# Kernel tuning notes

Measured on AMD Instinct MI355X. Metric: run time of the kernel, lower is better.

Reference implementation:

```python
import jax, jax.numpy as jnp
import numpy as np

N_NODES = 20000   # graph nodes (rows of x)
N_EDGES = 40000
NUM_ENT = 300000  # node_count: embedding table rows
EMB_DIM = 64
D = 2 * EMB_DIM           # self.emb_dim = 128
SE = int(0.36 * D)        # s_emb_dim = 46
TE = D - SE               # t_emb_dim = 82
F = 256                   # raw feature cols of x
HID = 128                 # n_hidden
OUT = 2


def setup_inputs() -> dict:
    key = jax.random.key(0)
    ks = jax.random.split(key, 24)
    def nrm(k, shape, fan_in):
        return jax.random.normal(k, shape, jnp.float32) / np.sqrt(fan_in)
    inp = {
        'x': jax.random.normal(ks[0], (N_NODES, F), jnp.float32),
        'heads': jax.random.randint(ks[1], (N_EDGES,), 0, NUM_ENT),
        'rels': jax.random.randint(ks[2], (N_EDGES,), 0, 4),
        'tails': jax.random.randint(ks[3], (N_EDGES,), 0, NUM_ENT),
        'weeks': jax.random.uniform(ks[4], (N_EDGES,), jnp.float32),
        'edge_src': jnp.sort(jax.random.randint(ks[5], (N_EDGES,), 0, N_NODES)),
        'edge_dst': jax.random.randint(ks[6], (N_EDGES,), 0, N_NODES),
        'node_type': jax.random.randint(ks[7], (N_NODES,), 0, 5),
        'edge_type': jax.random.randint(ks[8], (N_EDGES,), 0, 4),
        'edge_index': jax.random.randint(ks[9], (2, N_EDGES), 0, N_NODES),
        # learned parameters
        'ent_embs': nrm(ks[10], (NUM_ENT, SE), SE),
        'rel_embs': nrm(ks[11], (4, D), D),
        'w_freq': nrm(ks[12], (NUM_ENT, TE), TE),
        'w_phi': nrm(ks[13], (NUM_ENT, TE), TE),
        'w_amp': nrm(ks[14], (NUM_ENT, TE), TE),
        'Wih': nrm(ks[15], (4 * D, D), D),
        'Whh': nrm(ks[16], (4 * D, D), D),
        'bih': jnp.zeros((4 * D,), jnp.float32),
        'bhh': jnp.zeros((4 * D,), jnp.float32),
        'fc1_w': nrm(ks[17], (HID, F + D), F + D),
        'fc1_b': jnp.zeros((HID,), jnp.float32),
        'ln_g': jnp.ones((HID,), jnp.float32),
        'ln_b': jnp.zeros((HID,), jnp.float32),
        'out_w': nrm(ks[18], (OUT, HID), HID),
        'out_b': jnp.zeros((OUT,), jnp.float32),
    }
    return inp


def _lstm_last_per_segment(pre, seg, Whh, bhh):
    """Run one LSTM over edges sorted by seg, resetting state at group
    boundaries; return per-step hidden states and the scatter index that
    selects the last step of each group (others map to dummy row N_NODES).
    pre: [E, 4D] precomputed x @ Wih^T + bih (sorted by seg)."""
    reset = jnp.concatenate([jnp.ones((1,), bool), seg[1:] != seg[:-1]])
    def step(carry, inp):
        h, c = carry
        p, r = inp
        h = jnp.where(r, 0.0, h)
        c = jnp.where(r, 0.0, c)
        gates = p + h @ Whh.T + bhh
        i, f, g, o = jnp.split(gates, 4, axis=-1)
        c = jax.nn.sigmoid(f) * c + jax.nn.sigmoid(i) * jnp.tanh(g)
        h = jax.nn.sigmoid(o) * jnp.tanh(c)
        return (h, c), h
    zero = jnp.zeros((D,), pre.dtype)
    _, hs = jax.lax.scan(step, (zero, zero), (pre, reset))
    is_last = jnp.concatenate([seg[1:] != seg[:-1], jnp.ones((1,), bool)])
    idx = jnp.where(is_last, seg, N_NODES)  # dummy row for non-last steps
    return hs, idx


def reference(x, heads, rels, tails, weeks, edge_src, edge_dst, node_type,
              edge_type, edge_index, ent_embs, rel_embs, w_freq, w_phi, w_amp,
              Wih, Whh, bih, bhh, fc1_w, fc1_b, ln_g, ln_b, out_w, out_b):
    week = weeks.reshape(-1, 1)  # [E,1]
    # getEmbeddings: static entity emb + diachronic (amp*sin(freq*t+phi)) part
    h_t = w_amp[heads] * jnp.sin(w_freq[heads] * week + w_phi[heads])
    t_t = w_amp[tails] * jnp.sin(w_freq[tails] * week + w_phi[tails])
    h = jnp.concatenate([ent_embs[heads], h_t], axis=1)  # [E, D]
    t = jnp.concatenate([ent_embs[tails], t_t], axis=1)  # [E, D]
    r = rel_embs[rels]                                    # [E, D]
    scores = h * r * t                                    # [E, D]

    # Ragged per-group LSTM (src groups, then dst groups overwrite), fused
    # as a single segment-reset scan per pass. Input projection hoisted.
    pre = scores @ Wih.T + bih  # [E, 4D]
    emb = jnp.zeros((N_NODES + 1, D), scores.dtype)
    perm_s = jnp.argsort(edge_src)  # stable
    hs, idx = _lstm_last_per_segment(pre[perm_s], edge_src[perm_s], Whh, bhh)
    emb = emb.at[idx].set(hs)
    perm_d = jnp.argsort(edge_dst)
    hs, idx = _lstm_last_per_segment(pre[perm_d], edge_dst[perm_d], Whh, bhh)
    emb = emb.at[idx].set(hs)
    emb = emb[:N_NODES]

    # (hgtconv2 omitted: GeneralConv source unavailable; treated as identity)
    xc = jnp.concatenate([x, emb], axis=1)  # mask = arange(N): all rows
    h1 = xc @ fc1_w.T + fc1_b
    mu = jnp.mean(h1, axis=-1, keepdims=True)
    var = jnp.mean((h1 - mu) ** 2, axis=-1, keepdims=True)
    h1 = (h1 - mu) / jnp.sqrt(var + 1e-5) * ln_g + ln_b
    h1 = jax.nn.relu(h1)  # dropout: eval mode, identity
    return h1 @ out_w.T + out_b
```

## Files before the change

kernel.cpp:

```cpp
#include <hip/hip_runtime.h>
#include <math.h>

#define N_NODES 20000
#define N_EDGES 40000
#define SE 46
#define TE 82
#define NBLK 79

typedef short  s16x8 __attribute__((ext_vector_type(8)));
typedef short  s16x4 __attribute__((ext_vector_type(4)));
typedef float  f32x4 __attribute__((ext_vector_type(4)));

__device__ __forceinline__ float sigf(float x){ return 1.0f/(1.0f+__expf(-x)); }
__device__ __forceinline__ float tanh_f(float x){ return 1.0f - 2.0f/(__expf(2.0f*x)+1.0f); }
__device__ __forceinline__ int perm_out(int i){ return (i&3)*128 + (i>>2); }
__device__ __forceinline__ unsigned short f2bf(float f){
  unsigned u = __builtin_bit_cast(unsigned, f);
  unsigned r = (u + 0x7fff + ((u>>16)&1)) >> 16;
  return (unsigned short)r;
}
__device__ __forceinline__ float bf2f(short s){
  unsigned u = ((unsigned)(unsigned short)s) << 16;
  return __builtin_bit_cast(float, u);
}

#define GATHER_BLKS 2500
#define PREP_BLKS   704
#define HIST_BLKS   157
#define FRONT_BLKS  (GATHER_BLKS + PREP_BLKS + HIST_BLKS)

__global__ __launch_bounds__(256) void k_front(
    const int* __restrict__ heads, const int* __restrict__ rels,
    const int* __restrict__ tails, const float* __restrict__ weeks,
    const float* __restrict__ ent, const float* __restrict__ rel_embs,
    const float* __restrict__ wfreq, const float* __restrict__ wphi,
    const float* __restrict__ wamp, short* __restrict__ scores,
    const float* __restrict__ Wih, const float* __restrict__ Whh,
    const float* __restrict__ fc1w,
    short* __restrict__ WihB, short* __restrict__ WhhB2, short* __restrict__ fc1wbf,
    const int* __restrict__ esrc, const int* __restrict__ edst,
    int* __restrict__ scnt, int* __restrict__ dcnt){
  int blk = blockIdx.x, tid = threadIdx.x;
  if (blk < GATHER_BLKS){
    int c = blk*256 + tid;
    int e = c >> 4, d0 = (c & 15) << 3;
    int hd = heads[e], tl = tails[e], rl = rels[e];
    float wk = weeks[e];
    float hv[8], tv[8];
    if (d0 + 8 <= SE){
      const float* hp = ent + (size_t)hd*SE + d0;
      const float* tp = ent + (size_t)tl*SE + d0;
      #pragma unroll
      for (int j=0;j<4;j++){
        float2 a = *(const float2*)(hp + j*2); hv[2*j]=a.x; hv[2*j+1]=a.y;
        float2 b = *(const float2*)(tp + j*2); tv[2*j]=b.x; tv[2*j+1]=b.y;
      }
    } else if (d0 >= 48){
      int dt = d0 - SE;
      const float *hf = wfreq + (size_t)hd*TE + dt, *hp2 = wphi + (size_t)hd*TE + dt, *ha = wamp + (size_t)hd*TE + dt;
      const float *tf = wfreq + (size_t)tl*TE + dt, *tp2 = wphi + (size_t)tl*TE + dt, *ta = wamp + (size_t)tl*TE + dt;
      #pragma unroll
      for (int j=0;j<4;j++){
        float2 f_h = *(const float2*)(hf + j*2);
        float2 p_h = *(const float2*)(hp2 + j*2);
        float2 a_h = *(const float2*)(ha + j*2);
        float2 f_t = *(const float2*)(tf + j*2);
        float2 p_t = *(const float2*)(tp2 + j*2);
        float2 a_t = *(const float2*)(ta + j*2);
        hv[2*j]   = a_h.x*__sinf(f_h.x*wk + p_h.x);
        hv[2*j+1] = a_h.y*__sinf(f_h.y*wk + p_h.y);
        tv[2*j]   = a_t.x*__sinf(f_t.x*wk + p_t.x);
        tv[2*j+1] = a_t.y*__sinf(f_t.y*wk + p_t.y);
      }
    } else {
      #pragma unroll
      for (int j=0;j<8;j++){
        int d = 40 + j;
        if (d < SE){
          hv[j] = ent[(size_t)hd*SE + d];
          tv[j] = ent[(size_t)tl*SE + d];
        } else {
          int dt = d - SE;
          hv[j] = wamp[(size_t)hd*TE+dt]*__sinf(wfreq[(size_t)hd*TE+dt]*wk + wphi[(size_t)hd*TE+dt]);
          tv[j] = wamp[(size_t)tl*TE+dt]*__sinf(wfreq[(size_t)tl*TE+dt]*wk + wphi[(size_t)tl*TE+dt]);
        }
      }
    }
    const float* rp = rel_embs + rl*128 + d0;
    float4 r0 = *(const float4*)rp, r1 = *(const float4*)(rp+4);
    float rv[8] = {r0.x,r0.y,r0.z,r0.w, r1.x,r1.y,r1.z,r1.w};
    s16x8 o;
    #pragma unroll
    for (int j=0;j<8;j++) o[j] = (short)f2bf(hv[j]*rv[j]*tv[j]);
    *(s16x8*)(scores + (size_t)e*128 + d0) = o;
  } else if (blk < GATHER_BLKS + PREP_BLKS){
    int idx = (blk - GATHER_BLKS)*256 + tid;
    if (idx < 65536){
      int i = idx >> 7, k = idx & 127;
      WihB[idx] = (short)f2bf(Wih[perm_out(i)*128 + k]);
    } else if (idx < 131072){
      int j = idx - 65536;
      WhhB2[j] = (short)f2bf(Whh[j]);
    } else if (idx < 180224){
      int j = idx - 131072;
      fc1wbf[j] = (short)f2bf(fc1w[j]);
    }
  } else {
    int e = (blk - GATHER_BLKS - PREP_BLKS)*256 + tid;
    if (e < N_EDGES){ atomicAdd(&scnt[esrc[e]],1); atomicAdd(&dcnt[edst[e]],1); }
  }
}

__global__ __launch_bounds__(256) void k_pregemm(
    const short* __restrict__ scores, const short* __restrict__ WihB,
    const float* __restrict__ bih, const float* __restrict__ bhh,
    short* __restrict__ pre2b){
  __shared__ char As[32*256];
  int e0 = blockIdx.x * 32;
  int tid = threadIdx.x;
  #pragma unroll
  for (int q=0;q<2;q++){
    int c = tid + 256*q;
    int el = c >> 4, k8 = c & 15;
    s16x8 v = *(const s16x8*)(scores + (size_t)(e0+el)*128 + k8*8);
    *(s16x8*)(As + ((el*256 + k8*16) ^ ((el&7)<<4))) = v;
  }
  __syncthreads();
  int lane = tid & 63, w = tid >> 6;
  int cl = lane & 15, kq = lane >> 4;
  s16x8 a[2][4];
  #pragma unroll
  for (int ks=0;ks<4;ks++){
    int kb = ks*64 + kq*16;
    a[0][ks] = *(const s16x8*)(As + (((cl   )*256 + kb) ^ ((cl&7)<<4)));
    a[1][ks] = *(const s16x8*)(As + (((cl+16)*256 + kb) ^ (((cl+16)&7)<<4)));
  }
  f32x4 D[2][8];
  #pragma unroll
  for (int m=0;m<2;m++)
    #pragma unroll
    for (int i=0;i<8;i++) D[m][i] = (f32x4){0.f,0.f,0.f,0.f};
  #pragma unroll
  for (int i=0;i<8;i++){
    int n = w*128 + i*16 + cl;
    const short* bp = WihB + (size_t)n*128 + kq*8;
    #pragma unroll
    for (int ks=0;ks<4;ks++){
      s16x8 b = *(const s16x8*)(bp + ks*32);
      D[0][i] = __builtin_amdgcn_mfma_f32_16x16x32_bf16(a[0][ks], b, D[0][i], 0, 0, 0);
      D[1][i] = __builtin_amdgcn_mfma_f32_16x16x32_bf16(a[1][ks], b, D[1][i], 0, 0, 0);
    }
  }
  #pragma unroll
  for (int i=0;i<8;i++){
    int n = w*128 + i*16 + cl;
    int pn = perm_out(n);
    float bb = bih[pn] + bhh[pn];
    #pragma unroll
    for (int m=0;m<2;m++){
      #pragma unroll
      for (int q2=0;q2<4;q2++){
        int row = m*16 + kq*4 + q2;
        pre2b[(size_t)(e0+row)*512 + n] = (short)f2bf(D[m][i][q2] + bb);
      }
    }
  }
}

__global__ void k_scan(const int* __restrict__ scnt, const int* __restrict__ dcnt,
                       int* __restrict__ sstart, int* __restrict__ dstart){
  const int* cnt = blockIdx.x ? dcnt : scnt;
  int* start = blockIdx.x ? dstart : sstart;
  const int CH = 20;
  int tid = threadIdx.x;
  int base = tid*CH;
  int v[CH]; int tsum = 0;
  #pragma unroll
  for (int j=0;j<CH;j++){ int i = base+j; v[j] = (i<N_NODES)? cnt[i] : 0; tsum += v[j]; }
  int lane = tid & 63, wv = tid >> 6;
  int incl = tsum;
  #pragma unroll
  for (int m=1;m<64;m<<=1){ int u = __shfl_up(incl, m); if (lane >= m) incl += u; }
  __shared__ int wsum[16], woff[16];
  if (lane==63) wsum[wv] = incl;
  __syncthreads();
  if (tid < 16){ int s=0; for (int k=0;k<tid;k++) s += wsum[k]; woff[tid]=s; }
  __syncthreads();
  int run = woff[wv] + incl - tsum;
  #pragma unroll
  for (int j=0;j<CH;j++){ int i = base+j; if (i<N_NODES) start[i] = run; run += v[j]; }
  if (tid == 1023) start[N_NODES] = run;
}

__global__ __launch_bounds__(256) void k_scatcb1(
    const int* __restrict__ edst, const int* __restrict__ dstart,
    int* __restrict__ dc2, int* __restrict__ dlist,
    const int* __restrict__ sstart, int* __restrict__ bhist){
  int blk = blockIdx.x, tid = threadIdx.x;
  if (blk < HIST_BLKS){
    int e = blk*256 + tid;
    if (e < N_EDGES){
      int d = edst[e]; int p2 = dstart[d] + atomicAdd(&dc2[d],1); dlist[p2]=e;
    }
  } else {
    __shared__ int h[128];
    int b2 = blk - HIST_BLKS;
    if (tid < 128) h[tid] = 0;
    __syncthreads();
    int n = b2*256 + tid;
    if (n < N_NODES){
      int c  = sstart[n+1]-sstart[n];
      int c2 = dstart[n+1]-dstart[n];
      if (c>0 && c2==0) atomicAdd(&h[min(c,63)], 1);
      if (c2>0) atomicAdd(&h[64+min(c2,63)], 1);
    }
    __syncthreads();
    if (tid < 128) bhist[tid*NBLK + b2] = h[tid];
  }
}

__device__ __forceinline__ int mapbin(int s){
  int p = s / (63*NBLK);
  int r = s - p*63*NBLK;
  int li = r / NBLK;
  int b  = r - li*NBLK;
  int l  = 63 - li;
  return (p*64 + l)*NBLK + b;
}

__global__ __launch_bounds__(256) void k_sortcb2(
    const int* __restrict__ dstart, int* __restrict__ dlist,
    const int* __restrict__ bhist, int* __restrict__ boff,
    int* __restrict__ nchains){
  int blk = blockIdx.x, tid = threadIdx.x;
  __shared__ int wsum[4];
  __shared__ int pend[2];
  if (blk < NBLK){
    int n = blk*256 + tid;
    if (n < N_NODES){
      int a = dstart[n], b = dstart[n+1];
      for (int i=a+1;i<b;i++){
        int v = dlist[i]; int j=i-1;
        while (j>=a && dlist[j]>v){ dlist[j+1]=dlist[j]; j--; }
        dlist[j+1]=v;
      }
    }
  } else {
    const int S = 2*63*NBLK;
    const int CH2 = 39;
    int tsum = 0;
    for (int j=0;j<CH2;j++){
      int s = tid*CH2 + j;
      if (s < S) tsum += bhist[mapbin(s)];
    }
    int lane = tid & 63, wv = tid >> 6;
    int incl = tsum;
    #pragma unroll
    for (int m=1;m<64;m<<=1){ int u = __shfl_up(incl, m); if (lane >= m) incl += u; }
    if (lane==63) wsum[wv] = incl;
    __syncthreads();
    int woff = 0;
    for (int k=0;k<wv;k++) woff += wsum[k];
    int run = woff + incl - tsum;
    for (int j=0;j<CH2;j++){
      int s = tid*CH2 + j;
      if (s < S){
        int bi = mapbin(s);
        int val = bhist[bi];
        boff[bi] = run;
        run += val;
        if (s == 63*NBLK - 1) pend[0] = run;
        if (s == S - 1)       pend[1] = run;
      }
    }
    __syncthreads();
    if (tid == 0){
      nchains[0] = pend[0];
      nchains[1] = pend[1] - pend[0];
    }
  }
}

__global__ void k_cbin3(const int* __restrict__ sstart, const int* __restrict__ dstart,
                        const int* __restrict__ boff, const int* __restrict__ nchains,
                        int* __restrict__ cnode, int* __restrict__ cstart,
                        int* __restrict__ clen, int* __restrict__ degf){
  __shared__ int h[128];
  int tid = threadIdx.x, blk = blockIdx.x;
  if (tid < 128) h[tid] = 0;
  __syncthreads();
  int n = blk*256 + tid;
  int bin0=-1, bin1=-1, r0=0, r1=0, a0=0, c0=0, a1=0, c1=0;
  if (n < N_NODES){
    a0 = sstart[n]; c0 = sstart[n+1]-a0;
    a1 = dstart[n]; c1 = dstart[n+1]-a1;
    degf[n] = (c0+c1 > 0) ? 1 : 0;
    if (c0>0 && c1==0){ bin0 = min(c0,63);    r0 = atomicAdd(&h[bin0], 1); }
    if (c1>0)         { bin1 = 64+min(c1,63); r1 = atomicAdd(&h[bin1], 1); }
  }
  __syncthreads();
  int nch0 = nchains[0];
  if (bin0 >= 0){
    int pos = boff[bin0*NBLK + blk] + r0;
    cnode[pos] = n; cstart[pos] = a0; clen[pos] = c0;
  }
  if (bin1 >= 0){
    int pos = boff[bin1*NBLK + blk] + r1 - nch0;
    cnode[N_NODES+pos] = n; cstart[N_NODES+pos] = a1; clen[N_NODES+pos] = c1;
  }
}

__global__ __launch_bounds__(512, 1) void k_lstm7(
    const short* __restrict__ pre2b, const short* __restrict__ WhhB2,
    const int* __restrict__ cnode, const int* __restrict__ cstart,
    const int* __restrict__ clen, const int* __restrict__ nchains,
    const int* __restrict__ dlist, int* __restrict__ ctr,
    float* __restrict__ emb){
  __shared__ char Hb[2][8192];
  __shared__ int M[161];
  int tid = threadIdx.x;
  int lane = tid & 63, wv = tid >> 6;
  int cl = lane & 15, kq = lane >> 4;
  int d_own = wv*16 + cl;
  s16x8 wf[4][4];
  #pragma unroll
  for (int i=0;i<4;i++)
    #pragma unroll
    for (int ks=0;ks<4;ks++)
      wf[i][ks] = *(const s16x8*)(WhhB2 + (size_t)(i*128 + d_own)*128 + ks*32 + kq*8);
  int nch0 = nchains[0], nch1 = nchains[1];
  int B0 = (nch0+31)>>5, B1 = (nch1+31)>>5;
  while (true){
    if (tid==0) M[160] = atomicAdd(ctr, 1);
    __syncthreads();
    int nb = M[160];
    if (nb >= B0 + B1) break;
    int pass = (nb >= B0) ? 1 : 0;
    int batch = pass ? nb - B0 : nb;
    int b0 = batch << 5;
    int nch = pass ? nch1 : nch0;
    if (tid < 32){
      int j = b0 + tid;
      int valid = (j < nch);
      int ci = pass*N_NODES + j;
      int st = valid ? cstart[ci] : 0;
      int ln = valid ? clen[ci] : 0;
      M[tid] = ln; M[32+tid] = st; M[128+tid] = valid ? cnode[ci] : -1;
      M[64+tid] = (ln > 0) ? (pass ? dlist[st]   : st  ) : 0;
      M[96+tid] = (ln > 1) ? (pass ? dlist[st+1] : st+1) : 0;
    }
    *(unsigned long long*)(&Hb[0][tid*16])   = 0ull;
    *(unsigned long long*)(&Hb[0][tid*16+8]) = 0ull;
    float cst[8]  = {0.f,0.f,0.f,0.f,0.f,0.f,0.f,0.f};
    float hreg[8] = {0.f,0.f,0.f,0.f,0.f,0.f,0.f,0.f};
    __syncthreads();
    int mylen[8];
    #pragma unroll
    for (int m=0;m<2;m++)
      #pragma unroll
      for (int q=0;q<4;q++) mylen[m*4+q] = M[m*16 + kq*4 + q];
    int ml = 0;
    #pragma unroll 1
    for (int j=0;j<32;j++) ml = max(ml, M[j]);
    s16x4 pvc[8];
    #pragma unroll
    for (int m=0;m<2;m++)
      #pragma unroll
      for (int q=0;q<4;q++){
        int r = m*16 + kq*4 + q;
        pvc[m*4+q] = *(const s16x4*)(pre2b + (size_t)M[64+r]*512 + d_own*4);
      }
    __syncthreads();
    int cur = 0;
    for (int t=0; t<ml; t++){
      if (tid < 32){
        int ln = M[tid];
        int nxt = M[32+tid] + t + 2;
        M[64 + ((t&1)<<5) + tid] = (t+2 < ln) ? (pass ? dlist[nxt] : nxt) : 0;
      }
      s16x4 pvn[8];
      const int* eidN = M + 64 + (((t+1)&1)<<5);
      #pragma unroll
      for (int m=0;m<2;m++)
        #pragma unroll
        for (int q=0;q<4;q++){
          int r = m*16 + kq*4 + q;
          pvn[m*4+q] = *(const s16x4*)(pre2b + (size_t)eidN[r]*512 + d_own*4);
        }
      f32x4 D[2][4];
      #pragma unroll
      for (int m=0;m<2;m++)
        #pragma unroll
        for (int i=0;i<4;i++) D[m][i] = (f32x4){0.f,0.f,0.f,0.f};
      char* Hc = Hb[cur];
      #pragma unroll
      for (int ks=0; ks<4; ks++){
        int kb = ks*64 + kq*16;
        s16x8 a0 = *(const s16x8*)(Hc + (((cl   )*256 + kb) ^ ((cl&7)<<4)));
        s16x8 a1 = *(const s16x8*)(Hc + (((cl+16)*256 + kb) ^ (((cl+16)&7)<<4)));
        #pragma unroll
        for (int i=0;i<4;i++){
          D[0][i] = __builtin_amdgcn_mfma_f32_16x16x32_bf16(a0, wf[i][ks], D[0][i], 0, 0, 0);
          D[1][i] = __builtin_amdgcn_mfma_f32_16x16x32_bf16(a1, wf[i][ks], D[1][i], 0, 0, 0);
        }
      }
      char* Hn = Hb[cur^1];
      #pragma unroll
      for (int m=0;m<2;m++)
        #pragma unroll
        for (int q=0;q<4;q++){
          int r = m*16 + kq*4 + q;
          if (t < mylen[m*4+q]){
            s16x4 p = pvc[m*4+q];
            float gi = D[m][0][q] + bf2f(p[0]);
            float gf = D[m][1][q] + bf2f(p[1]);
            float gg = D[m][2][q] + bf2f(p[2]);
            float go = D[m][3][q] + bf2f(p[3]);
            int idx = m*4+q;
            cst[idx] = sigf(gf)*cst[idx] + sigf(gi)*tanh_f(gg);
            float h = sigf(go)*tanh_f(cst[idx]);
            hreg[idx] = h;
            *(short*)(Hn + ((r*256 + d_own*2) ^ ((r&7)<<4))) = (short)f2bf(h);
          }
        }
      __syncthreads();
      #pragma unroll
      for (int i=0;i<8;i++) pvc[i] = pvn[i];
      cur ^= 1;
    }
    #pragma unroll
    for (int m=0;m<2;m++)
      #pragma unroll
      for (int q=0;q<4;q++){
        int r = m*16 + kq*4 + q;
        int n = M[128+r];
        if (mylen[m*4+q] > 0 && n >= 0){
          emb[(size_t)n*128 + d_own] = hreg[m*4+q];
        }
      }
    __syncthreads();
  }
}

__global__ __launch_bounds__(512) void k_mlp2(
    const float* __restrict__ x, const float* __restrict__ emb,
    const int* __restrict__ degf,
    const short* __restrict__ fc1wbf, const float* __restrict__ fc1b,
    const float* __restrict__ lng, const float* __restrict__ lnb,
    const float* __restrict__ outw, const float* __restrict__ outb,
    float* __restrict__ out){
  __shared__ char As[32*768];
  __shared__ float hbuf[32][132];
  int tid = threadIdx.x;
  int lane = tid & 63, w = tid >> 6;
  int base = blockIdx.x * 32;
  #pragma unroll
  for (int q=0;q<3;q++){
    int i = tid + 512*q;
    int r = i / 48, c = i - r*48;
    s16x8 v8 = {0,0,0,0,0,0,0,0};
    if (c < 32){
      const float* src = x + (size_t)(base+r)*256 + c*8;
      float4 v0 = *(const float4*)src;
      float4 v1 = *(const float4*)(src+4);
      v8[0]=(short)f2bf(v0.x); v8[1]=(short)f2bf(v0.y); v8[2]=(short)f2bf(v0.z); v8[3]=(short)f2bf(v0.w);
      v8[4]=(short)f2bf(v1.x); v8[5]=(short)f2bf(v1.y); v8[6]=(short)f2bf(v1.z); v8[7]=(short)f2bf(v1.w);
    } else if (degf[base+r]){
      const float* src = emb + (size_t)(base+r)*128 + (c-32)*8;
      float4 v0 = *(const float4*)src;
      float4 v1 = *(const float4*)(src+4);
      v8[0]=(short)f2bf(v0.x); v8[1]=(short)f2bf(v0.y); v8[2]=(short)f2bf(v0.z); v8[3]=(short)f2bf(v0.w);
      v8[4]=(short)f2bf(v1.x); v8[5]=(short)f2bf(v1.y); v8[6]=(short)f2bf(v1.z); v8[7]=(short)f2bf(v1.w);
    }
    *(s16x8*)(As + ((r*768 + c*16) ^ ((r&7)<<4))) = v8;
  }
  __syncthreads();
  int cl = lane & 15, kq = lane >> 4;
  f32x4 D0 = {0.f,0.f,0.f,0.f}, D1 = {0.f,0.f,0.f,0.f};
  const short* bp = fc1wbf + (size_t)(w*16 + cl)*384 + kq*8;
  #pragma unroll
  for (int ks=0; ks<12; ks++){
    s16x8 b = *(const s16x8*)(bp + ks*32);
    int kb = ks*64 + kq*16;
    s16x8 a0 = *(const s16x8*)(As + (((cl   )*768 + kb) ^ ((cl&7)<<4)));
    s16x8 a1 = *(const s16x8*)(As + (((cl+16)*768 + kb) ^ (((cl+16)&7)<<4)));
    D0 = __builtin_amdgcn_mfma_f32_16x16x32_bf16(a0, b, D0, 0, 0, 0);
    D1 = __builtin_amdgcn_mfma_f32_16x16x32_bf16(a1, b, D1, 0, 0, 0);
  }
  int col = w*16 + cl;
  float bb = fc1b[col];
  #pragma unroll
  for (int q=0;q<4;q++){
    hbuf[kq*4+q][col]    = D0[q] + bb;
    hbuf[16+kq*4+q][col] = D1[q] + bb;
  }
  __syncthreads();
  int sub = lane >> 4, l16 = lane & 15;
  int nd = w*4 + sub;
  float v[8];
  float s = 0.f;
  #pragma unroll
  for (int j=0;j<8;j++){ v[j] = hbuf[nd][l16*8+j]; s += v[j]; }
  #pragma unroll
  for (int m=1;m<16;m<<=1) s += __shfl_xor(s, m);
  float mu = s * (1.f/128.f);
  float va = 0.f;
  #pragma unroll
  for (int j=0;j<8;j++){ float dm = v[j]-mu; va += dm*dm; }
  #pragma unroll
  for (int m=1;m<16;m<<=1) va += __shfl_xor(va, m);
  float rstd = rsqrtf(va*(1.f/128.f) + 1e-5f);
  float o0=0.f, o1=0.f;
  #pragma unroll
  for (int j=0;j<8;j++){
    int c = l16*8+j;
    float h1 = (v[j]-mu)*rstd*lng[c] + lnb[c];
    h1 = fmaxf(h1, 0.f);
    o0 += h1*outw[c]; o1 += h1*outw[128+c];
  }
  #pragma unroll
  for (int m=1;m<16;m<<=1){ o0 += __shfl_xor(o0,m); o1 += __shfl_xor(o1,m); }
  if (l16==0){
    out[(size_t)(base+nd)*2]   = o0 + outb[0];
    out[(size_t)(base+nd)*2+1] = o1 + outb[1];
  }
}

extern "C" void kernel_launch(void* const* d_in, const int* in_sizes, int n_in,
                              void* d_out, int out_size, void* d_ws, size_t ws_size,
                              hipStream_t stream){
  const float* x      = (const float*)d_in[0];
  const int*   heads  = (const int*)d_in[1];
  const int*   rels   = (const int*)d_in[2];
  const int*   tails  = (const int*)d_in[3];
  const float* weeks  = (const float*)d_in[4];
  const int*   esrc   = (const int*)d_in[5];
  const int*   edst   = (const int*)d_in[6];
  const float* ent    = (const float*)d_in[10];
  const float* rel_e  = (const float*)d_in[11];
  const float* wfreq  = (const float*)d_in[12];
  const float* wphi   = (const float*)d_in[13];
  const float* wamp   = (const float*)d_in[14];
  const float* Wih    = (const float*)d_in[15];
  const float* Whh    = (const float*)d_in[16];
  const float* bih    = (const float*)d_in[17];
  const float* bhh    = (const float*)d_in[18];
  const float* fc1w   = (const float*)d_in[19];
  const float* fc1b   = (const float*)d_in[20];
  const float* lng    = (const float*)d_in[21];
  const float* lnb    = (const float*)d_in[22];
  const float* outw   = (const float*)d_in[23];
  const float* outb   = (const float*)d_in[24];
  float* out = (float*)d_out;

  char* ws = (char*)d_ws;
  size_t off = 0;
  auto alloc = [&](size_t bytes){ void* p = ws + off; off += (bytes + 255) & ~(size_t)255; return p; };
  short* pre2b  = (short*)alloc((size_t)N_EDGES*512*2);
  short* scores = (short*)alloc((size_t)N_EDGES*128*2);
  short* WihB   = (short*)alloc(512*128*2);
  short* WhhB2  = (short*)alloc(512*128*2);
  short* fc1wbf = (short*)alloc(128*384*2);
  float* emb    = (float*)alloc((size_t)N_NODES*128*4);
  int* sstart   = (int*)alloc((N_NODES+1)*4);
  int* dstart   = (int*)alloc((N_NODES+1)*4);
  int* zreg     = (int*)alloc((size_t)(3*N_NODES + 3)*4);
  int* scnt = zreg, *dcnt = zreg+N_NODES, *dc2 = zreg+2*N_NODES;
  int* nchains  = zreg + 3*N_NODES;
  int* ctr      = nchains + 2;
  int* bhist    = (int*)alloc((size_t)128*NBLK*4);
  int* boff     = (int*)alloc((size_t)128*NBLK*4);
  int* dlist    = (int*)alloc(N_EDGES*4);
  int* cnode    = (int*)alloc((size_t)2*N_NODES*4);
  int* cstart   = (int*)alloc((size_t)2*N_NODES*4);
  int* clen     = (int*)alloc((size_t)2*N_NODES*4);
  int* degf     = (int*)alloc((size_t)N_NODES*4);

  hipMemsetAsync(zreg, 0, (size_t)(3*N_NODES + 3)*4, stream);

  k_front<<<FRONT_BLKS, 256, 0, stream>>>(heads, rels, tails, weeks, ent, rel_e,
                                          wfreq, wphi, wamp, scores,
                                          Wih, Whh, fc1w, WihB, WhhB2, fc1wbf,
                                          esrc, edst, scnt, dcnt);
  k_pregemm<<<N_EDGES/32, 256, 0, stream>>>(scores, WihB, bih, bhh, pre2b);
  k_scan<<<2, 1024, 0, stream>>>(scnt, dcnt, sstart, dstart);
  k_scatcb1<<<HIST_BLKS + NBLK, 256, 0, stream>>>(edst, dstart, dc2, dlist, sstart, bhist);
  k_sortcb2<<<NBLK + 1, 256, 0, stream>>>(dstart, dlist, bhist, boff, nchains);
  k_cbin3<<<NBLK, 256, 0, stream>>>(sstart, dstart, boff, nchains, cnode, cstart, clen, degf);
  k_lstm7<<<256, 512, 0, stream>>>(pre2b, WhhB2, cnode, cstart, clen, nchains,
                                   dlist, ctr, emb);
  k_mlp2<<<N_NODES/32, 512, 0, stream>>>(x, emb, degf, fc1wbf, fc1b, lng, lnb, outw, outb, out);
}
```

Measured before the change: 170.4 us.

## Fuse all pipeline stages into one cooperative persistent kernel with grid syncs

Replaces the eight separate kernel launches (front gather, pre-GEMM, scan, scatter/histogram, sort, binning, LSTM, MLP) with a single cooperative kernel of 256 blocks of 512 threads that separates phases with grid.sync. The aim is to remove per-launch overhead and idle gaps between the many small dependent stages. Work in each phase is redistributed with grid-stride loops, and the scan and histogram layouts are reworked (NB2 bins, overlapping the scan with the pre-GEMM). The cost is heavier grid-wide barriers, fixed occupancy of 2 blocks per CU, and lower parallelism in phases that used to launch thousands of blocks.

New measurement: 380.2 us. 123% more time.

```diff
diff --git a/kernel.cpp b/kernel.cpp
--- a/kernel.cpp
+++ b/kernel.cpp
@@ -1,11 +1,15 @@
 #include <hip/hip_runtime.h>
+#include <hip/hip_cooperative_groups.h>
 #include <math.h>
+
+namespace cg = cooperative_groups;
 
 #define N_NODES 20000
 #define N_EDGES 40000
 #define SE 46
 #define TE 82
-#define NBLK 79
+#define NB2 80
+#define TT  131072
 
 typedef short  s16x8 __attribute__((ext_vector_type(8)));
 typedef short  s16x4 __attribute__((ext_vector_type(4)));
@@ -23,33 +27,41 @@
   unsigned u = ((unsigned)(unsigned short)s) << 16;
   return __builtin_bit_cast(float, u);
 }
-
-#define GATHER_BLKS 2500
-#define PREP_BLKS   704
-#define HIST_BLKS   157
-#define FRONT_BLKS  (GATHER_BLKS + PREP_BLKS + HIST_BLKS)
-
-__global__ __launch_bounds__(256) void k_front(
-    const int* __restrict__ heads, const int* __restrict__ rels,
-    const int* __restrict__ tails, const float* __restrict__ weeks,
-    const float* __restrict__ ent, const float* __restrict__ rel_embs,
-    const float* __restrict__ wfreq, const float* __restrict__ wphi,
-    const float* __restrict__ wamp, short* __restrict__ scores,
-    const float* __restrict__ Wih, const float* __restrict__ Whh,
-    const float* __restrict__ fc1w,
-    short* __restrict__ WihB, short* __restrict__ WhhB2, short* __restrict__ fc1wbf,
-    const int* __restrict__ esrc, const int* __restrict__ edst,
-    int* __restrict__ scnt, int* __restrict__ dcnt){
-  int blk = blockIdx.x, tid = threadIdx.x;
-  if (blk < GATHER_BLKS){
-    int c = blk*256 + tid;
+__device__ __forceinline__ int mapbin(int s){
+  int p = s / (63*NB2);
+  int r = s - p*(63*NB2);
+  int li = r / NB2;
+  int b  = r - li*NB2;
+  int l  = 63 - li;
+  return (p*64 + l)*NB2 + b;
+}
+
+struct MegaParams {
+  const int *heads, *rels, *tails;
+  const float *weeks, *ent, *rel_embs, *wfreq, *wphi, *wamp;
+  const int *esrc, *edst;
+  const float *x, *Wih, *Whh, *fc1w, *bih, *bhh, *fc1b, *lng, *lnb, *outw, *outb;
+  float *out;
+  short *scores, *WihB, *WhhB2, *fc1wbf, *pre2b;
+  float *emb;
+  int *sstart, *dstart, *scnt, *dcnt, *dc2, *nchains, *ctr;
+  int *bhist, *boff, *dlist, *cnode, *cstart, *clen, *degf;
+};
+
+__global__ __launch_bounds__(512, 2) void k_mega(MegaParams P){
+  __shared__ char SM[41472];
+  cg::grid_group grid = cg::this_grid();
+  int tid = threadIdx.x, blk = blockIdx.x;
+  int gid = blk*512 + tid;
+
+  for (int c = gid; c < N_EDGES*16; c += TT){
     int e = c >> 4, d0 = (c & 15) << 3;
-    int hd = heads[e], tl = tails[e], rl = rels[e];
-    float wk = weeks[e];
+    int hd = P.heads[e], tl = P.tails[e], rl = P.rels[e];
+    float wk = P.weeks[e];
     float hv[8], tv[8];
     if (d0 + 8 <= SE){
-      const float* hp = ent + (size_t)hd*SE + d0;
-      const float* tp = ent + (size_t)tl*SE + d0;
+      const float* hp = P.ent + (size_t)hd*SE + d0;
+      const float* tp = P.ent + (size_t)tl*SE + d0;
       #pragma unroll
       for (int j=0;j<4;j++){
         float2 a = *(const float2*)(hp + j*2); hv[2*j]=a.x; hv[2*j+1]=a.y;
@@ -57,8 +69,8 @@
       }
     } else if (d0 >= 48){
       int dt = d0 - SE;
-      const float *hf = wfreq + (size_t)hd*TE + dt, *hp2 = wphi + (size_t)hd*TE + dt, *ha = wamp + (size_t)hd*TE + dt;
-      const float *tf = wfreq + (size_t)tl*TE + dt, *tp2 = wphi + (size_t)tl*TE + dt, *ta = wamp + (size_t)tl*TE + dt;
+      const float *hf = P.wfreq + (size_t)hd*TE + dt, *hp2 = P.wphi + (size_t)hd*TE + dt, *ha = P.wamp + (size_t)hd*TE + dt;
+      const float *tf = P.wfreq + (size_t)tl*TE + dt, *tp2 = P.wphi + (size_t)tl*TE + dt, *ta = P.wamp + (size_t)tl*TE + dt;
       #pragma unroll
       for (int j=0;j<4;j++){
         float2 f_h = *(const float2*)(hf + j*2);
@@ -77,482 +89,435 @@
       for (int j=0;j<8;j++){
         int d = 40 + j;
         if (d < SE){
-          hv[j] = ent[(size_t)hd*SE + d];
-          tv[j] = ent[(size_t)tl*SE + d];
+          hv[j] = P.ent[(size_t)hd*SE + d];
+          tv[j] = P.ent[(size_t)tl*SE + d];
         } else {
           int dt = d - SE;
-          hv[j] = wamp[(size_t)hd*TE+dt]*__sinf(wfreq[(size_t)hd*TE+dt]*wk + wphi[(size_t)hd*TE+dt]);
-          tv[j] = wamp[(size_t)tl*TE+dt]*__sinf(wfreq[(size_t)tl*TE+dt]*wk + wphi[(size_t)tl*TE+dt]);
-        }
-      }
-    }
-    const float* rp = rel_embs + rl*128 + d0;
+          hv[j] = P.wamp[(size_t)hd*TE+dt]*__sinf(P.wfreq[(size_t)hd*TE+dt]*wk + P.wphi[(size_t)hd*TE+dt]);
+          tv[j] = P.wamp[(size_t)tl*TE+dt]*__sinf(P.wfreq[(size_t)tl*TE+dt]*wk + P.wphi[(size_t)tl*TE+dt]);
+        }
+      }
+    }
+    const float* rp = P.rel_embs + rl*128 + d0;
     float4 r0 = *(const float4*)rp, r1 = *(const float4*)(rp+4);
     float rv[8] = {r0.x,r0.y,r0.z,r0.w, r1.x,r1.y,r1.z,r1.w};
     s16x8 o;
     #pragma unroll
     for (int j=0;j<8;j++) o[j] = (short)f2bf(hv[j]*rv[j]*tv[j]);
-    *(s16x8*)(scores + (size_t)e*128 + d0) = o;
-  } else if (blk < GATHER_BLKS + PREP_BLKS){
-    int idx = (blk - GATHER_BLKS)*256 + tid;
-    if (idx < 65536){
-      int i = idx >> 7, k = idx & 127;
-      WihB[idx] = (short)f2bf(Wih[perm_out(i)*128 + k]);
-    } else if (idx < 131072){
-      int j = idx - 65536;
-      WhhB2[j] = (short)f2bf(Whh[j]);
-    } else if (idx < 180224){
-      int j = idx - 131072;
-      fc1wbf[j] = (short)f2bf(fc1w[j]);
-    }
+    *(s16x8*)(P.scores + (size_t)e*128 + d0) = o;
+  }
+  for (int i = gid; i < 180224; i += TT){
+    if (i < 65536){
+      int r = i >> 7, k = i & 127;
+      P.WihB[i] = (short)f2bf(P.Wih[perm_out(r)*128 + k]);
+    } else if (i < 131072){
+      int j = i - 65536;
+      P.WhhB2[j] = (short)f2bf(P.Whh[j]);
+    } else {
+      int j = i - 131072;
+      P.fc1wbf[j] = (short)f2bf(P.fc1w[j]);
+    }
+  }
+  if (gid < N_EDGES){ atomicAdd(&P.scnt[P.esrc[gid]],1); atomicAdd(&P.dcnt[P.edst[gid]],1); }
+  grid.sync();
+
+  if (blk == 0){
+    int half = tid >> 8, t = tid & 255;
+    const int* cnt = half ? P.dcnt : P.scnt;
+    int* start = half ? P.dstart : P.sstart;
+    int base = t*79;
+    int lim = min(base+79, N_NODES);
+    int tsum = 0;
+    for (int i=base;i<lim;i++) tsum += cnt[i];
+    int lane = tid & 63;
+    int wv4 = t >> 6;
+    int incl = tsum;
+    #pragma unroll
+    for (int m=1;m<64;m<<=1){ int u = __shfl_up(incl, m); if (lane >= m) incl += u; }
+    int* wsA = (int*)SM;
+    if (lane == 63) wsA[half*4 + wv4] = incl;
+    __syncthreads();
+    int woff = 0;
+    for (int k=0;k<wv4;k++) woff += wsA[half*4 + k];
+    int run = woff + incl - tsum;
+    for (int i=base;i<lim;i++){ start[i] = run; run += cnt[i]; }
+    if (t == 255) start[N_NODES] = run;
   } else {
-    int e = (blk - GATHER_BLKS - PREP_BLKS)*256 + tid;
-    if (e < N_EDGES){ atomicAdd(&scnt[esrc[e]],1); atomicAdd(&dcnt[edst[e]],1); }
-  }
-}
-
-__global__ __launch_bounds__(256) void k_pregemm(
-    const short* __restrict__ scores, const short* __restrict__ WihB,
-    const float* __restrict__ bih, const float* __restrict__ bhh,
-    short* __restrict__ pre2b){
-  __shared__ char As[32*256];
-  int e0 = blockIdx.x * 32;
-  int tid = threadIdx.x;
-  #pragma unroll
-  for (int q=0;q<2;q++){
-    int c = tid + 256*q;
-    int el = c >> 4, k8 = c & 15;
-    s16x8 v = *(const s16x8*)(scores + (size_t)(e0+el)*128 + k8*8);
-    *(s16x8*)(As + ((el*256 + k8*16) ^ ((el&7)<<4))) = v;
-  }
-  __syncthreads();
-  int lane = tid & 63, w = tid >> 6;
-  int cl = lane & 15, kq = lane >> 4;
-  s16x8 a[2][4];
-  #pragma unroll
-  for (int ks=0;ks<4;ks++){
-    int kb = ks*64 + kq*16;
-    a[0][ks] = *(const s16x8*)(As + (((cl   )*256 + kb) ^ ((cl&7)<<4)));
-    a[1][ks] = *(const s16x8*)(As + (((cl+16)*256 + kb) ^ (((cl+16)&7)<<4)));
-  }
-  f32x4 D[2][8];
-  #pragma unroll
-  for (int m=0;m<2;m++)
-    #pragma unroll
-    for (int i=0;i<8;i++) D[m][i] = (f32x4){0.f,0.f,0.f,0.f};
-  #pragma unroll
-  for (int i=0;i<8;i++){
-    int n = w*128 + i*16 + cl;
-    const short* bp = WihB + (size_t)n*128 + kq*8;
-    #pragma unroll
-    for (int ks=0;ks<4;ks++){
-      s16x8 b = *(const s16x8*)(bp + ks*32);
-      D[0][i] = __builtin_amdgcn_mfma_f32_16x16x32_bf16(a[0][ks], b, D[0][i], 0, 0, 0);
-      D[1][i] = __builtin_amdgcn_mfma_f32_16x16x32_bf16(a[1][ks], b, D[1][i], 0, 0, 0);
-    }
-  }
-  #pragma unroll
-  for (int i=0;i<8;i++){
-    int n = w*128 + i*16 + cl;
-    int pn = perm_out(n);
-    float bb = bih[pn] + bhh[pn];
-    #pragma unroll
-    for (int m=0;m<2;m++){
-      #pragma unroll
-      for (int q2=0;q2<4;q2++){
-        int row = m*16 + kq*4 + q2;
-        pre2b[(size_t)(e0+row)*512 + n] = (short)f2bf(D[m][i][q2] + bb);
-      }
-    }
-  }
-}
-
-__global__ void k_scan(const int* __restrict__ scnt, const int* __restrict__ dcnt,
-                       int* __restrict__ sstart, int* __restrict__ dstart){
-  const int* cnt = blockIdx.x ? dcnt : scnt;
-  int* start = blockIdx.x ? dstart : sstart;
-  const int CH = 20;
-  int tid = threadIdx.x;
-  int base = tid*CH;
-  int v[CH]; int tsum = 0;
-  #pragma unroll
-  for (int j=0;j<CH;j++){ int i = base+j; v[j] = (i<N_NODES)? cnt[i] : 0; tsum += v[j]; }
-  int lane = tid & 63, wv = tid >> 6;
-  int incl = tsum;
-  #pragma unroll
-  for (int m=1;m<64;m<<=1){ int u = __shfl_up(incl, m); if (lane >= m) incl += u; }
-  __shared__ int wsum[16], woff[16];
-  if (lane==63) wsum[wv] = incl;
-  __syncthreads();
-  if (tid < 16){ int s=0; for (int k=0;k<tid;k++) s += wsum[k]; woff[tid]=s; }
-  __syncthreads();
-  int run = woff[wv] + incl - tsum;
-  #pragma unroll
-  for (int j=0;j<CH;j++){ int i = base+j; if (i<N_NODES) start[i] = run; run += v[j]; }
-  if (tid == 1023) start[N_NODES] = run;
-}
-
-__global__ __launch_bounds__(256) void k_scatcb1(
-    const int* __restrict__ edst, const int* __restrict__ dstart,
-    int* __restrict__ dc2, int* __restrict__ dlist,
-    const int* __restrict__ sstart, int* __restrict__ bhist){
-  int blk = blockIdx.x, tid = threadIdx.x;
-  if (blk < HIST_BLKS){
-    int e = blk*256 + tid;
-    if (e < N_EDGES){
-      int d = edst[e]; int p2 = dstart[d] + atomicAdd(&dc2[d],1); dlist[p2]=e;
-    }
-  } else {
-    __shared__ int h[128];
-    int b2 = blk - HIST_BLKS;
-    if (tid < 128) h[tid] = 0;
-    __syncthreads();
-    int n = b2*256 + tid;
+    int half = tid >> 8, t = tid & 255;
+    char* As = SM + half*8192;
+    for (int rnd=0; rnd<3; rnd++){
+      int tile = rnd*510 + (blk-1)*2 + half;
+      bool act = (tile < 1250);
+      int e0 = tile*32;
+      if (act){
+        #pragma unroll
+        for (int q=0;q<2;q++){
+          int c = t + 256*q;
+          int el = c >> 4, k8 = c & 15;
+          s16x8 v = *(const s16x8*)(P.scores + (size_t)(e0+el)*128 + k8*8);
+          *(s16x8*)(As + ((el*256 + k8*16) ^ ((el&7)<<4))) = v;
+        }
+      }
+      __syncthreads();
+      if (act){
+        int lane = t & 63, w = t >> 6;
+        int cl = lane & 15, kq = lane >> 4;
+        s16x8 a[2][4];
+        #pragma unroll
+        for (int ks=0;ks<4;ks++){
+          int kb = ks*64 + kq*16;
+          a[0][ks] = *(const s16x8*)(As + (((cl   )*256 + kb) ^ ((cl&7)<<4)));
+          a[1][ks] = *(const s16x8*)(As + (((cl+16)*256 + kb) ^ (((cl+16)&7)<<4)));
+        }
+        f32x4 D[2][8];
+        #pragma unroll
+        for (int m=0;m<2;m++)
+          #pragma unroll
+          for (int i=0;i<8;i++) D[m][i] = (f32x4){0.f,0.f,0.f,0.f};
+        #pragma unroll
+        for (int i=0;i<8;i++){
+          int n = w*128 + i*16 + cl;
+          const short* bp = P.WihB + (size_t)n*128 + kq*8;
+          #pragma unroll
+          for (int ks=0;ks<4;ks++){
+            s16x8 b = *(const s16x8*)(bp + ks*32);
+            D[0][i] = __builtin_amdgcn_mfma_f32_16x16x32_bf16(a[0][ks], b, D[0][i], 0, 0, 0);
+            D[1][i] = __builtin_amdgcn_mfma_f32_16x16x32_bf16(a[1][ks], b, D[1][i], 0, 0, 0);
+          }
+        }
+        #pragma unroll
+        for (int i=0;i<8;i++){
+          int n = w*128 + i*16 + cl;
+          int pn = perm_out(n);
+          float bb = P.bih[pn] + P.bhh[pn];
+          #pragma unroll
+          for (int m=0;m<2;m++){
+            #pragma unroll
+            for (int q2=0;q2<4;q2++){
+              int row = m*16 + kq*4 + q2;
+              P.pre2b[(size_t)(e0+row)*512 + n] = (short)f2bf(D[m][i][q2] + bb);
+            }
+          }
+        }
+      }
+      __syncthreads();
+    }
+  }
+  grid.sync();
+
+  if (gid < N_EDGES){
+    int d = P.edst[gid];
+    int p2 = P.dstart[d] + atomicAdd(&P.dc2[d],1);
+    P.dlist[p2] = gid;
+  }
+  if (blk < 40){
+    int half = tid >> 8, t = tid & 255;
+    int* h = (int*)SM + half*128;
+    if (t < 128) h[t] = 0;
+    __syncthreads();
+    int vb = blk*2 + half;
+    int n = vb*256 + t;
     if (n < N_NODES){
-      int c  = sstart[n+1]-sstart[n];
-      int c2 = dstart[n+1]-dstart[n];
-      if (c>0 && c2==0) atomicAdd(&h[min(c,63)], 1);
-      if (c2>0) atomicAdd(&h[64+min(c2,63)], 1);
-    }
-    __syncthreads();
-    if (tid < 128) bhist[tid*NBLK + b2] = h[tid];
-  }
-}
-
-__device__ __forceinline__ int mapbin(int s){
-  int p = s / (63*NBLK);
-  int r = s - p*63*NBLK;
-  int li = r / NBLK;
-  int b  = r - li*NBLK;
-  int l  = 63 - li;
-  return (p*64 + l)*NBLK + b;
-}
-
-__global__ __launch_bounds__(256) void k_sortcb2(
-    const int* __restrict__ dstart, int* __restrict__ dlist,
-    const int* __restrict__ bhist, int* __restrict__ boff,
-    int* __restrict__ nchains){
-  int blk = blockIdx.x, tid = threadIdx.x;
-  __shared__ int wsum[4];
-  __shared__ int pend[2];
-  if (blk < NBLK){
-    int n = blk*256 + tid;
-    if (n < N_NODES){
-      int a = dstart[n], b = dstart[n+1];
-      for (int i=a+1;i<b;i++){
-        int v = dlist[i]; int j=i-1;
-        while (j>=a && dlist[j]>v){ dlist[j+1]=dlist[j]; j--; }
-        dlist[j+1]=v;
-      }
-    }
-  } else {
-    const int S = 2*63*NBLK;
-    const int CH2 = 39;
+      int c0 = P.sstart[n+1]-P.sstart[n];
+      int c1 = P.dstart[n+1]-P.dstart[n];
+      P.degf[n] = (c0+c1 > 0) ? 1 : 0;
+      if (c0>0 && c1==0) atomicAdd(&h[min(c0,63)], 1);
+      if (c1>0) atomicAdd(&h[64+min(c1,63)], 1);
+    }
+    __syncthreads();
+    if (t < 128) P.bhist[t*NB2 + vb] = h[t];
+  }
+  grid.sync();
+
+  if (gid < N_NODES){
+    int a = P.dstart[gid], b = P.dstart[gid+1];
+    for (int i=a+1;i<b;i++){
+      int v = P.dlist[i]; int j=i-1;
+      while (j>=a && P.dlist[j]>v){ P.dlist[j+1]=P.dlist[j]; j--; }
+      P.dlist[j+1]=v;
+    }
+  }
+  if (blk == 0){
+    const int S = 2*63*NB2;
+    const int CH2 = 20;
     int tsum = 0;
     for (int j=0;j<CH2;j++){
       int s = tid*CH2 + j;
-      if (s < S) tsum += bhist[mapbin(s)];
+      if (s < S) tsum += P.bhist[mapbin(s)];
     }
     int lane = tid & 63, wv = tid >> 6;
     int incl = tsum;
     #pragma unroll
     for (int m=1;m<64;m<<=1){ int u = __shfl_up(incl, m); if (lane >= m) incl += u; }
-    if (lane==63) wsum[wv] = incl;
+    int* ws = (int*)SM;
+    int* pend = (int*)SM + 16;
+    if (lane==63) ws[wv] = incl;
     __syncthreads();
     int woff = 0;
-    for (int k=0;k<wv;k++) woff += wsum[k];
+    for (int k=0;k<wv;k++) woff += ws[k];
     int run = woff + incl - tsum;
     for (int j=0;j<CH2;j++){
       int s = tid*CH2 + j;
       if (s < S){
         int bi = mapbin(s);
-        int val = bhist[bi];
-        boff[bi] = run;
+        int val = P.bhist[bi];
+        P.boff[bi] = run;
         run += val;
-        if (s == 63*NBLK - 1) pend[0] = run;
-        if (s == S - 1)       pend[1] = run;
-      }
-    }
-    __syncthreads();
-    if (tid == 0){
-      nchains[0] = pend[0];
-      nchains[1] = pend[1] - pend[0];
-    }
-  }
-}
-
-__global__ void k_cbin3(const int* __restrict__ sstart, const int* __restrict__ dstart,
-                        const int* __restrict__ boff, const int* __restrict__ nchains,
-                        int* __restrict__ cnode, int* __restrict__ cstart,
-                        int* __restrict__ clen, int* __restrict__ degf){
-  __shared__ int h[128];
-  int tid = threadIdx.x, blk = blockIdx.x;
-  if (tid < 128) h[tid] = 0;
-  __syncthreads();
-  int n = blk*256 + tid;
-  int bin0=-1, bin1=-1, r0=0, r1=0, a0=0, c0=0, a1=0, c1=0;
-  if (n < N_NODES){
-    a0 = sstart[n]; c0 = sstart[n+1]-a0;
-    a1 = dstart[n]; c1 = dstart[n+1]-a1;
-    degf[n] = (c0+c1 > 0) ? 1 : 0;
-    if (c0>0 && c1==0){ bin0 = min(c0,63);    r0 = atomicAdd(&h[bin0], 1); }
-    if (c1>0)         { bin1 = 64+min(c1,63); r1 = atomicAdd(&h[bin1], 1); }
-  }
-  __syncthreads();
-  int nch0 = nchains[0];
-  if (bin0 >= 0){
-    int pos = boff[bin0*NBLK + blk] + r0;
-    cnode[pos] = n; cstart[pos] = a0; clen[pos] = c0;
-  }
-  if (bin1 >= 0){
-    int pos = boff[bin1*NBLK + blk] + r1 - nch0;
-    cnode[N_NODES+pos] = n; cstart[N_NODES+pos] = a1; clen[N_NODES+pos] = c1;
-  }
-}
-
-__global__ __launch_bounds__(512, 1) void k_lstm7(
-    const short* __restrict__ pre2b, const short* __restrict__ WhhB2,
-    const int* __restrict__ cnode, const int* __restrict__ cstart,
-    const int* __restrict__ clen, const int* __restrict__ nchains,
-    const int* __restrict__ dlist, int* __restrict__ ctr,
-    float* __restrict__ emb){
-  __shared__ char Hb[2][8192];
-  __shared__ int M[161];
-  int tid = threadIdx.x;
-  int lane = tid & 63, wv = tid >> 6;
-  int cl = lane & 15, kq = lane >> 4;
-  int d_own = wv*16 + cl;
-  s16x8 wf[4][4];
-  #pragma unroll
-  for (int i=0;i<4;i++)
+        if (s == 63*NB2 - 1) pend[0] = run;
+        if (s == S - 1)      pend[1] = run;
+      }
+    }
+    __syncthreads();
+    if (tid == 0){ P.nchains[0] = pend[0]; P.nchains[1] = pend[1] - pend[0]; }
+  }
+  grid.sync();
+
+  if (blk < 40){
+    int half = tid >> 8, t = tid & 255;
+    int* h = (int*)SM + half*128;
+    if (t < 128) h[t] = 0;
+    __syncthreads();
+    int vb = blk*2 + half;
+    int n = vb*256 + t;
+    int bin0=-1, bin1=-1, r0=0, r1=0, a0=0, c0=0, a1=0, c1=0;
+    if (n < N_NODES){
+      a0 = P.sstart[n]; c0 = P.sstart[n+1]-a0;
+      a1 = P.dstart[n]; c1 = P.dstart[n+1]-a1;
+      if (c0>0 && c1==0){ bin0 = min(c0,63);    r0 = atomicAdd(&h[bin0],1); }
+      if (c1>0)         { bin1 = 64+min(c1,63); r1 = atomicAdd(&h[bin1],1); }
+    }
+    __syncthreads();
+    int nch0 = P.nchains[0];
+    if (bin0 >= 0){
+      int pos = P.boff[bin0*NB2 + vb] + r0;
+      P.cnode[pos]=n; P.cstart[pos]=a0; P.clen[pos]=c0;
+    }
+    if (bin1 >= 0){
+      int pos = P.boff[bin1*NB2 + vb] + r1 - nch0;
+      P.cnode[N_NODES+pos]=n; P.cstart[N_NODES+pos]=a1; P.clen[N_NODES+pos]=c1;
+    }
+  }
+  grid.sync();
+
+  {
+    char* Hb0 = SM;
+    int* M = (int*)(SM + 16384);
+    int lane = tid & 63, wv = tid >> 6;
+    int cl = lane & 15, kq = lane >> 4;
+    int d_own = wv*16 + cl;
+    s16x8 wf[4][4];
     #pragma unroll
-    for (int ks=0;ks<4;ks++)
-      wf[i][ks] = *(const s16x8*)(WhhB2 + (size_t)(i*128 + d_own)*128 + ks*32 + kq*8);
-  int nch0 = nchains[0], nch1 = nchains[1];
-  int B0 = (nch0+31)>>5, B1 = (nch1+31)>>5;
-  while (true){
-    if (tid==0) M[160] = atomicAdd(ctr, 1);
-    __syncthreads();
-    int nb = M[160];
-    if (nb >= B0 + B1) break;
-    int pass = (nb >= B0) ? 1 : 0;
-    int batch = pass ? nb - B0 : nb;
-    int b0 = batch << 5;
-    int nch = pass ? nch1 : nch0;
-    if (tid < 32){
-      int j = b0 + tid;
-      int valid = (j < nch);
-      int ci = pass*N_NODES + j;
-      int st = valid ? cstart[ci] : 0;
-      int ln = valid ? clen[ci] : 0;
-      M[tid] = ln; M[32+tid] = st; M[128+tid] = valid ? cnode[ci] : -1;
-      M[64+tid] = (ln > 0) ? (pass ? dlist[st]   : st  ) : 0;
-      M[96+tid] = (ln > 1) ? (pass ? dlist[st+1] : st+1) : 0;
-    }
-    *(unsigned long long*)(&Hb[0][tid*16])   = 0ull;
-    *(unsigned long long*)(&Hb[0][tid*16+8]) = 0ull;
-    float cst[8]  = {0.f,0.f,0.f,0.f,0.f,0.f,0.f,0.f};
-    float hreg[8] = {0.f,0.f,0.f,0.f,0.f,0.f,0.f,0.f};
-    __syncthreads();
-    int mylen[8];
-    #pragma unroll
-    for (int m=0;m<2;m++)
-      #pragma unroll
-      for (int q=0;q<4;q++) mylen[m*4+q] = M[m*16 + kq*4 + q];
-    int ml = 0;
-    #pragma unroll 1
-    for (int j=0;j<32;j++) ml = max(ml, M[j]);
-    s16x4 pvc[8];
-    #pragma unroll
-    for (int m=0;m<2;m++)
-      #pragma unroll
-      for (int q=0;q<4;q++){
-        int r = m*16 + kq*4 + q;
-        pvc[m*4+q] = *(const s16x4*)(pre2b + (size_t)M[64+r]*512 + d_own*4);
-      }
-    __syncthreads();
-    int cur = 0;
-    for (int t=0; t<ml; t++){
+    for (int i=0;i<4;i++)
+      #pragma unroll
+      for (int ks=0;ks<4;ks++)
+        wf[i][ks] = *(const s16x8*)(P.WhhB2 + (size_t)(i*128 + d_own)*128 + ks*32 + kq*8);
+    int nch0 = P.nchains[0], nch1 = P.nchains[1];
+    int B0 = (nch0+31)>>5, B1 = (nch1+31)>>5;
+    while (true){
+      if (tid==0) M[160] = atomicAdd(P.ctr, 1);
+      __syncthreads();
+      int nb = M[160];
+      if (nb >= B0 + B1) break;
+      int pass = (nb >= B0) ? 1 : 0;
+      int batch = pass ? nb - B0 : nb;
+      int b0 = batch << 5;
+      int nch = pass ? nch1 : nch0;
       if (tid < 32){
-        int ln = M[tid];
-        int nxt = M[32+tid] + t + 2;
-        M[64 + ((t&1)<<5) + tid] = (t+2 < ln) ? (pass ? dlist[nxt] : nxt) : 0;
-      }
-      s16x4 pvn[8];
-      const int* eidN = M + 64 + (((t+1)&1)<<5);
+        int j = b0 + tid;
+        int valid = (j < nch);
+        int ci = pass*N_NODES + j;
+        int st = valid ? P.cstart[ci] : 0;
+        int ln = valid ? P.clen[ci] : 0;
+        M[tid] = ln; M[32+tid] = st; M[128+tid] = valid ? P.cnode[ci] : -1;
+        M[64+tid] = (ln > 0) ? (pass ? P.dlist[st]   : st  ) : 0;
+        M[96+tid] = (ln > 1) ? (pass ? P.dlist[st+1] : st+1) : 0;
+      }
+      *(unsigned long long*)(&Hb0[tid*16])   = 0ull;
+      *(unsigned long long*)(&Hb0[tid*16+8]) = 0ull;
+      float cst[8]  = {0.f,0.f,0.f,0.f,0.f,0.f,0.f,0.f};
+      float hreg[8] = {0.f,0.f,0.f,0.f,0.f,0.f,0.f,0.f};
+      __syncthreads();
+      int mylen[8];
+      #pragma unroll
+      for (int m=0;m<2;m++)
+        #pragma unroll
+        for (int q=0;q<4;q++) mylen[m*4+q] = M[m*16 + kq*4 + q];
+      int ml = 0;
+      #pragma unroll 1
+      for (int j=0;j<32;j++) ml = max(ml, M[j]);
+      s16x4 pvc[8];
       #pragma unroll
       for (int m=0;m<2;m++)
         #pragma unroll
         for (int q=0;q<4;q++){
           int r = m*16 + kq*4 + q;
-          pvn[m*4+q] = *(const s16x4*)(pre2b + (size_t)eidN[r]*512 + d_own*4);
-        }
-      f32x4 D[2][4];
-      #pragma unroll
-      for (int m=0;m<2;m++)
-        #pragma unroll
-        for (int i=0;i<4;i++) D[m][i] = (f32x4){0.f,0.f,0.f,0.f};
-      char* Hc = Hb[cur];
-      #pragma unroll
-      for (int ks=0; ks<4; ks++){
-        int kb = ks*64 + kq*16;
-        s16x8 a0 = *(const s16x8*)(Hc + (((cl   )*256 + kb) ^ ((cl&7)<<4)));
-        s16x8 a1 = *(const s16x8*)(Hc + (((cl+16)*256 + kb) ^ (((cl+16)&7)<<4)));
-        #pragma unroll
-        for (int i=0;i<4;i++){
-          D[0][i] = __builtin_amdgcn_mfma_f32_16x16x32_bf16(a0, wf[i][ks], D[0][i], 0, 0, 0);
-          D[1][i] = __builtin_amdgcn_mfma_f32_16x16x32_bf16(a1, wf[i][ks], D[1][i], 0, 0, 0);
-        }
-      }
-      char* Hn = Hb[cur^1];
+          pvc[m*4+q] = *(const s16x4*)(P.pre2b + (size_t)M[64+r]*512 + d_own*4);
+        }
+      __syncthreads();
+      int cur = 0;
+      for (int t=0; t<ml; t++){
+        if (tid < 32){
+          int ln = M[tid];
+          int nxt = M[32+tid] + t + 2;
+          M[64 + ((t&1)<<5) + tid] = (t+2 < ln) ? (pass ? P.dlist[nxt] : nxt) : 0;
+        }
+        s16x4 pvn[8];
+        const int* eidN = M + 64 + (((t+1)&1)<<5);
+        #pragma unroll
+        for (int m=0;m<2;m++)
+          #pragma unroll
+          for (int q=0;q<4;q++){
+            int r = m*16 + kq*4 + q;
+            pvn[m*4+q] = *(const s16x4*)(P.pre2b + (size_t)eidN[r]*512 + d_own*4);
+          }
+        f32x4 D[2][4];
+        #pragma unroll
+        for (int m=0;m<2;m++)
+          #pragma unroll
+          for (int i=0;i<4;i++) D[m][i] = (f32x4){0.f,0.f,0.f,0.f};
+        char* Hc = Hb0 + cur*8192;
+        #pragma unroll
+        for (int ks=0; ks<4; ks++){
+          int kb = ks*64 + kq*16;
+          s16x8 a0 = *(const s16x8*)(Hc + (((cl   )*256 + kb) ^ ((cl&7)<<4)));
+          s16x8 a1 = *(const s16x8*)(Hc + (((cl+16)*256 + kb) ^ (((cl+16)&7)<<4)));
+          #pragma unroll
+          for (int i=0;i<4;i++){
+            D[0][i] = __builtin_amdgcn_mfma_f32_16x16x32_bf16(a0, wf[i][ks], D[0][i], 0, 0, 0);
+            D[1][i] = __builtin_amdgcn_mfma_f32_16x16x32_bf16(a1, wf[i][ks], D[1][i], 0, 0, 0);
+          }
+        }
+        char* Hn = Hb0 + (cur^1)*8192;
+        #pragma unroll
+        for (int m=0;m<2;m++)
+          #pragma unroll
+          for (int q=0;q<4;q++){
+            int r = m*16 + kq*4 + q;
+            if (t < mylen[m*4+q]){
+              s16x4 p = pvc[m*4+q];
+              float gi = D[m][0][q] + bf2f(p[0]);
+              float gf = D[m][1][q] + bf2f(p[1]);
+              float gg = D[m][2][q] + bf2f(p[2]);
+              float go = D[m][3][q] + bf2f(p[3]);
+              int idx = m*4+q;
+              cst[idx] = sigf(gf)*cst[idx] + sigf(gi)*tanh_f(gg);
+              float h = sigf(go)*tanh_f(cst[idx]);
+              hreg[idx] = h;
+              *(short*)(Hn + ((r*256 + d_own*2) ^ ((r&7)<<4))) = (short)f2bf(h);
+            }
+          }
+        __syncthreads();
+        #pragma unroll
+        for (int i=0;i<8;i++) pvc[i] = pvn[i];
+        cur ^= 1;
+      }
       #pragma unroll
       for (int m=0;m<2;m++)
         #pragma unroll
         for (int q=0;q<4;q++){
           int r = m*16 + kq*4 + q;
-          if (t < mylen[m*4+q]){
-            s16x4 p = pvc[m*4+q];
-            float gi = D[m][0][q] + bf2f(p[0]);
-            float gf = D[m][1][q] + bf2f(p[1]);
-            float gg = D[m][2][q] + bf2f(p[2]);
-            float go = D[m][3][q] + bf2f(p[3]);
-            int idx = m*4+q;
-            cst[idx] = sigf(gf)*cst[idx] + sigf(gi)*tanh_f(gg);
-            float h = sigf(go)*tanh_f(cst[idx]);
-            hreg[idx] = h;
-            *(short*)(Hn + ((r*256 + d_own*2) ^ ((r&7)<<4))) = (short)f2bf(h);
-          }
-        }
-      __syncthreads();
-      #pragma unroll
-      for (int i=0;i<8;i++) pvc[i] = pvn[i];
-      cur ^= 1;
-    }
-    #pragma unroll
-    for (int m=0;m<2;m++)
-      #pragma unroll
-      for (int q=0;q<4;q++){
-        int r = m*16 + kq*4 + q;
-        int n = M[128+r];
-        if (mylen[m*4+q] > 0 && n >= 0){
-          emb[(size_t)n*128 + d_own] = hreg[m*4+q];
-        }
-      }
-    __syncthreads();
-  }
-}
-
-__global__ __launch_bounds__(512) void k_mlp2(
-    const float* __restrict__ x, const float* __restrict__ emb,
-    const int* __restrict__ degf,
-    const short* __restrict__ fc1wbf, const float* __restrict__ fc1b,
-    const float* __restrict__ lng, const float* __restrict__ lnb,
-    const float* __restrict__ outw, const float* __restrict__ outb,
-    float* __restrict__ out){
-  __shared__ char As[32*768];
-  __shared__ float hbuf[32][132];
-  int tid = threadIdx.x;
-  int lane = tid & 63, w = tid >> 6;
-  int base = blockIdx.x * 32;
-  #pragma unroll
-  for (int q=0;q<3;q++){
-    int i = tid + 512*q;
-    int r = i / 48, c = i - r*48;
-    s16x8 v8 = {0,0,0,0,0,0,0,0};
-    if (c < 32){
-      const float* src = x + (size_t)(base+r)*256 + c*8;
-      float4 v0 = *(const float4*)src;
-      float4 v1 = *(const float4*)(src+4);
-      v8[0]=(short)f2bf(v0.x); v8[1]=(short)f2bf(v0.y); v8[2]=(short)f2bf(v0.z); v8[3]=(short)f2bf(v0.w);
-      v8[4]=(short)f2bf(v1.x); v8[5]=(short)f2bf(v1.y); v8[6]=(short)f2bf(v1.z); v8[7]=(short)f2bf(v1.w);
-    } else if (degf[base+r]){
-      const float* src = emb + (size_t)(base+r)*128 + (c-32)*8;
-      float4 v0 = *(const float4*)src;
-      float4 v1 = *(const float4*)(src+4);
-      v8[0]=(short)f2bf(v0.x); v8[1]=(short)f2bf(v0.y); v8[2]=(short)f2bf(v0.z); v8[3]=(short)f2bf(v0.w);
-      v8[4]=(short)f2bf(v1.x); v8[5]=(short)f2bf(v1.y); v8[6]=(short)f2bf(v1.z); v8[7]=(short)f2bf(v1.w);
-    }
-    *(s16x8*)(As + ((r*768 + c*16) ^ ((r&7)<<4))) = v8;
-  }
-  __syncthreads();
-  int cl = lane & 15, kq = lane >> 4;
-  f32x4 D0 = {0.f,0.f,0.f,0.f}, D1 = {0.f,0.f,0.f,0.f};
-  const short* bp = fc1wbf + (size_t)(w*16 + cl)*384 + kq*8;
-  #pragma unroll
-  for (int ks=0; ks<12; ks++){
-    s16x8 b = *(const s16x8*)(bp + ks*32);
-    int kb = ks*64 + kq*16;
-    s16x8 a0 = *(const s16x8*)(As + (((cl   )*768 + kb) ^ ((cl&7)<<4)));
-    s16x8 a1 = *(const s16x8*)(As + (((cl+16)*768 + kb) ^ (((cl+16)&7)<<4)));
-    D0 = __builtin_amdgcn_mfma_f32_16x16x32_bf16(a0, b, D0, 0, 0, 0);
-    D1 = __builtin_amdgcn_mfma_f32_16x16x32_bf16(a1, b, D1, 0, 0, 0);
-  }
-  int col = w*16 + cl;
-  float bb = fc1b[col];
-  #pragma unroll
-  for (int q=0;q<4;q++){
-    hbuf[kq*4+q][col]    = D0[q] + bb;
-    hbuf[16+kq*4+q][col] = D1[q] + bb;
-  }
-  __syncthreads();
-  int sub = lane >> 4, l16 = lane & 15;
-  int nd = w*4 + sub;
-  float v[8];
-  float s = 0.f;
-  #pragma unroll
-  for (int j=0;j<8;j++){ v[j] = hbuf[nd][l16*8+j]; s += v[j]; }
-  #pragma unroll
-  for (int m=1;m<16;m<<=1) s += __shfl_xor(s, m);
-  float mu = s * (1.f/128.f);
-  float va = 0.f;
-  #pragma unroll
-  for (int j=0;j<8;j++){ float dm = v[j]-mu; va += dm*dm; }
-  #pragma unroll
-  for (int m=1;m<16;m<<=1) va += __shfl_xor(va, m);
-  float rstd = rsqrtf(va*(1.f/128.f) + 1e-5f);
-  float o0=0.f, o1=0.f;
-  #pragma unroll
-  for (int j=0;j<8;j++){
-    int c = l16*8+j;
-    float h1 = (v[j]-mu)*rstd*lng[c] + lnb[c];
-    h1 = fmaxf(h1, 0.f);
-    o0 += h1*outw[c]; o1 += h1*outw[128+c];
-  }
-  #pragma unroll
-  for (int m=1;m<16;m<<=1){ o0 += __shfl_xor(o0,m); o1 += __shfl_xor(o1,m); }
-  if (l16==0){
-    out[(size_t)(base+nd)*2]   = o0 + outb[0];
-    out[(size_t)(base+nd)*2+1] = o1 + outb[1];
+          int n = M[128+r];
+          if (mylen[m*4+q] > 0 && n >= 0){
+            P.emb[(size_t)n*128 + d_own] = hreg[m*4+q];
+          }
+        }
+      __syncthreads();
+    }
+  }
+  grid.sync();
+
+  {
+    char* As = SM;
+    float (*hbuf)[132] = (float(*)[132])(SM + 24576);
+    int lane = tid & 63, w = tid >> 6;
+    for (int rnd=0; rnd<3; rnd++){
+      int tile = blk + 256*rnd;
+      bool act = (tile < 625);
+      int base = tile*32;
+      if (act){
+        #pragma unroll
+        for (int q=0;q<3;q++){
+          int i = tid + 512*q;
+          int r = i / 48, c2 = i - r*48;
+          s16x8 v8 = {0,0,0,0,0,0,0,0};
+          if (c2 < 32){
+            const float* src = P.x + (size_t)(base+r)*256 + c2*8;
+            float4 v0 = *(const float4*)src;
+            float4 v1 = *(const float4*)(src+4);
+            v8[0]=(short)f2bf(v0.x); v8[1]=(short)f2bf(v0.y); v8[2]=(short)f2bf(v0.z); v8[3]=(short)f2bf(v0.w);
+            v8[4]=(short)f2bf(v1.x); v8[5]=(short)f2bf(v1.y); v8[6]=(short)f2bf(v1.z); v8[7]=(short)f2bf(v1.w);
+          } else if (P.degf[base+r]){
+            const float* src = P.emb + (size_t)(base+r)*128 + (c2-32)*8;
+            float4 v0 = *(const float4*)src;
+            float4 v1 = *(const float4*)(src+4);
+            v8[0]=(short)f2bf(v0.x); v8[1]=(short)f2bf(v0.y); v8[2]=(short)f2bf(v0.z); v8[3]=(short)f2bf(v0.w);
+            v8[4]=(short)f2bf(v1.x); v8[5]=(short)f2bf(v1.y); v8[6]=(short)f2bf(v1.z); v8[7]=(short)f2bf(v1.w);
+          }
+          *(s16x8*)(As + ((r*768 + c2*16) ^ ((r&7)<<4))) = v8;
+        }
+      }
+      __syncthreads();
+      int cl = lane & 15, kq = lane >> 4;
+      if (act){
+        f32x4 D0 = {0.f,0.f,0.f,0.f}, D1 = {0.f,0.f,0.f,0.f};
+        const short* bp = P.fc1wbf + (size_t)(w*16 + cl)*384 + kq*8;
+        #pragma unroll
+        for (int ks=0; ks<12; ks++){
+          s16x8 b = *(const s16x8*)(bp + ks*32);
+          int kb = ks*64 + kq*16;
+          s16x8 a0 = *(const s16x8*)(As + (((cl   )*768 + kb) ^ ((cl&7)<<4)));
+          s16x8 a1 = *(const s16x8*)(As + (((cl+16)*768 + kb) ^ (((cl+16)&7)<<4)));
+          D0 = __builtin_amdgcn_mfma_f32_16x16x32_bf16(a0, b, D0, 0, 0, 0);
+          D1 = __builtin_amdgcn_mfma_f32_16x16x32_bf16(a1, b, D1, 0, 0, 0);
+        }
+        int col = w*16 + cl;
+        float bb = P.fc1b[col];
+        #pragma unroll
+        for (int q=0;q<4;q++){
+          hbuf[kq*4+q][col]    = D0[q] + bb;
+          hbuf[16+kq*4+q][col] = D1[q] + bb;
+        }
+      }
+      __syncthreads();
+      if (act){
+        int sub = lane >> 4, l16 = lane & 15;
+        int nd = w*4 + sub;
+        float v[8];
+        float s = 0.f;
+        #pragma unroll
+        for (int j=0;j<8;j++){ v[j] = hbuf[nd][l16*8+j]; s += v[j]; }
+        #pragma unroll
+        for (int m=1;m<16;m<<=1) s += __shfl_xor(s, m);
+        float mu = s * (1.f/128.f);
+        float va = 0.f;
+        #pragma unroll
+        for (int j=0;j<8;j++){ float dm = v[j]-mu; va += dm*dm; }
+        #pragma unroll
+        for (int m=1;m<16;m<<=1) va += __shfl_xor(va, m);
+        float rstd = rsqrtf(va*(1.f/128.f) + 1e-5f);
+        float o0=0.f, o1=0.f;
+        #pragma unroll
+        for (int j=0;j<8;j++){
+          int c = l16*8+j;
+          float h1 = (v[j]-mu)*rstd*P.lng[c] + P.lnb[c];
+          h1 = fmaxf(h1, 0.f);
+          o0 += h1*P.outw[c]; o1 += h1*P.outw[128+c];
+        }
+        #pragma unroll
+        for (int m=1;m<16;m<<=1){ o0 += __shfl_xor(o0,m); o1 += __shfl_xor(o1,m); }
+        if (l16==0){
+          P.out[(size_t)(base+nd)*2]   = o0 + P.outb[0];
+          P.out[(size_t)(base+nd)*2+1] = o1 + P.outb[1];
+        }
+      }
+      __syncthreads();
+    }
   }
 }
 
 extern "C" void kernel_launch(void* const* d_in, const int* in_sizes, int n_in,
                               void* d_out, int out_size, void* d_ws, size_t ws_size,
                               hipStream_t stream){
-  const float* x      = (const float*)d_in[0];
-  const int*   heads  = (const int*)d_in[1];
-  const int*   rels   = (const int*)d_in[2];
-  const int*   tails  = (const int*)d_in[3];
-  const float* weeks  = (const float*)d_in[4];
-  const int*   esrc   = (const int*)d_in[5];
-  const int*   edst   = (const int*)d_in[6];
-  const float* ent    = (const float*)d_in[10];
-  const float* rel_e  = (const float*)d_in[11];
-  const float* wfreq  = (const float*)d_in[12];
-  const float* wphi   = (const float*)d_in[13];
-  const float* wamp   = (const float*)d_in[14];
-  const float* Wih    = (const float*)d_in[15];
-  const float* Whh    = (const float*)d_in[16];
-  const float* bih    = (const float*)d_in[17];
-  const float* bhh    = (const float*)d_in[18];
-  const float* fc1w   = (const float*)d_in[19];
-  const float* fc1b   = (const float*)d_in[20];
-  const float* lng    = (const float*)d_in[21];
-  const float* lnb    = (const float*)d_in[22];
-  const float* outw   = (const float*)d_in[23];
-  const float* outb   = (const float*)d_in[24];
-  float* out = (float*)d_out;
-
   char* ws = (char*)d_ws;
   size_t off = 0;
   auto alloc = [&](size_t bytes){ void* p = ws + off; off += (bytes + 255) & ~(size_t)255; return p; };
@@ -568,8 +533,8 @@
   int* scnt = zreg, *dcnt = zreg+N_NODES, *dc2 = zreg+2*N_NODES;
   int* nchains  = zreg + 3*N_NODES;
   int* ctr      = nchains + 2;
-  int* bhist    = (int*)alloc((size_t)128*NBLK*4);
-  int* boff     = (int*)alloc((size_t)128*NBLK*4);
+  int* bhist    = (int*)alloc((size_t)128*NB2*4);
+  int* boff     = (int*)alloc((size_t)128*NB2*4);
   int* dlist    = (int*)alloc(N_EDGES*4);
   int* cnode    = (int*)alloc((size_t)2*N_NODES*4);
   int* cstart   = (int*)alloc((size_t)2*N_NODES*4);
@@ -578,16 +543,38 @@
 
   hipMemsetAsync(zreg, 0, (size_t)(3*N_NODES + 3)*4, stream);
 
-  k_front<<<FRONT_BLKS, 256, 0, stream>>>(heads, rels, tails, weeks, ent, rel_e,
-                                          wfreq, wphi, wamp, scores,
-                                          Wih, Whh, fc1w, WihB, WhhB2, fc1wbf,
-                                          esrc, edst, scnt, dcnt);
-  k_pregemm<<<N_EDGES/32, 256, 0, stream>>>(scores, WihB, bih, bhh, pre2b);
-  k_scan<<<2, 1024, 0, stream>>>(scnt, dcnt, sstart, dstart);
-  k_scatcb1<<<HIST_BLKS + NBLK, 256, 0, stream>>>(edst, dstart, dc2, dlist, sstart, bhist);
-  k_sortcb2<<<NBLK + 1, 256, 0, stream>>>(dstart, dlist, bhist, boff, nchains);
-  k_cbin3<<<NBLK, 256, 0, stream>>>(sstart, dstart, boff, nchains, cnode, cstart, clen, degf);
-  k_lstm7<<<256, 512, 0, stream>>>(pre2b, WhhB2, cnode, cstart, clen, nchains,
-                                   dlist, ctr, emb);
-  k_mlp2<<<N_NODES/32, 512, 0, stream>>>(x, emb, degf, fc1wbf, fc1b, lng, lnb, outw, outb, out);
+  MegaParams mp;
+  mp.heads = (const int*)d_in[1];
+  mp.rels  = (const int*)d_in[2];
+  mp.tails = (const int*)d_in[3];
+  mp.weeks = (const float*)d_in[4];
+  mp.ent   = (const float*)d_in[10];
+  mp.rel_embs = (const float*)d_in[11];
+  mp.wfreq = (const float*)d_in[12];
+  mp.wphi  = (const float*)d_in[13];
+  mp.wamp  = (const float*)d_in[14];
+  mp.esrc  = (const int*)d_in[5];
+  mp.edst  = (const int*)d_in[6];
+  mp.x     = (const float*)d_in[0];
+  mp.Wih   = (const float*)d_in[15];
+  mp.Whh   = (const float*)d_in[16];
+  mp.fc1w  = (const float*)d_in[19];
+  mp.bih   = (const float*)d_in[17];
+  mp.bhh   = (const float*)d_in[18];
+  mp.fc1b  = (const float*)d_in[20];
+  mp.lng   = (const float*)d_in[21];
+  mp.lnb   = (const float*)d_in[22];
+  mp.outw  = (const float*)d_in[23];
+  mp.outb  = (const float*)d_in[24];
+  mp.out   = (float*)d_out;
+  mp.scores = scores; mp.WihB = WihB; mp.WhhB2 = WhhB2; mp.fc1wbf = fc1wbf;
+  mp.pre2b = pre2b; mp.emb = emb;
+  mp.sstart = sstart; mp.dstart = dstart;
+  mp.scnt = scnt; mp.dcnt = dcnt; mp.dc2 = dc2;
+  mp.nchains = nchains; mp.ctr = ctr;
+  mp.bhist = bhist; mp.boff = boff; mp.dlist = dlist;
+  mp.cnode = cnode; mp.cstart = cstart; mp.clen = clen; mp.degf = degf;
+
+  void* args[] = { &mp };
+  hipLaunchCooperativeKernel((const void*)k_mega, dim3(256), dim3(512), args, 0, stream);
 }
```
